# Kernel tuning notes

Measured on AMD Instinct MI355X. Metric: run time of the kernel, lower is better.

## Reference

```python
import jax, jax.numpy as jnp
import numpy as np

NEG_SLOPE = 0.2  # LeakyReLU slope

N, E, D_IN, D_OUT, H, NBIN = 50000, 500000, 256, 256, 8, 10
DH = D_OUT // H


def setup_inputs() -> dict:
    key = jax.random.key(0)
    ks = jax.random.split(key, 9)
    emb_rel = jax.random.normal(ks[0], (N, D_IN), dtype=jnp.float32)
    head_idxs = jax.random.randint(ks[1], (E,), 0, N, dtype=jnp.int32)
    tail_idxs = jax.random.randint(ks[2], (E,), 0, N, dtype=jnp.int32)
    bins = jax.random.randint(ks[3], (E,), 0, NBIN, dtype=jnp.int32)
    # xavier-normal-ish scaled params (gain for relu)
    attn_proj_w = jax.random.normal(ks[4], (D_OUT, 2 * D_IN), dtype=jnp.float32) * (1.4142 * (2.0 / (2 * D_IN + D_OUT)) ** 0.5)
    attn_proj_b = jnp.zeros((D_OUT,), dtype=jnp.float32)
    attn_bin = jax.random.normal(ks[5], (NBIN, H, 1), dtype=jnp.float32) * 0.3
    attn_vec = jax.random.normal(ks[6], (1, H, DH), dtype=jnp.float32) * (1.4142 * (2.0 / (H + DH)) ** 0.5)
    aggr_proj_w = jax.random.normal(ks[7], (D_OUT, D_IN), dtype=jnp.float32) * (1.4142 * (2.0 / (D_IN + D_OUT)) ** 0.5)
    aggr_proj_b = jnp.zeros((D_OUT,), dtype=jnp.float32)
    return {
        "emb_rel": emb_rel,
        "head_idxs": head_idxs,
        "tail_idxs": tail_idxs,
        "bins": bins,
        "attn_proj_w": attn_proj_w,
        "attn_proj_b": attn_proj_b,
        "attn_bin": attn_bin,
        "attn_vec": attn_vec,
        "aggr_proj_w": aggr_proj_w,
        "aggr_proj_b": aggr_proj_b,
        "num_nodes": N,
    }


def reference(emb_rel, head_idxs, tail_idxs, bins, attn_proj_w, attn_proj_b,
              attn_bin, attn_vec, aggr_proj_w, aggr_proj_b, num_nodes):
    num_head, dim_hid = attn_vec.shape[1], attn_vec.shape[2]
    eh = emb_rel[head_idxs]                      # (E, D_in)
    et = emb_rel[tail_idxs]                      # (E, D_in)
    concat = jnp.concatenate([eh, et], axis=-1)  # (E, 2*D_in)
    proj = (concat @ attn_proj_w.T + attn_proj_b).reshape(-1, num_head, dim_hid)
    lrelu = jnp.where(proj >= 0, proj, NEG_SLOPE * proj)
    # raw attention logits per edge/head: (E, H, 1)
    attn_raw = jnp.sum(lrelu * attn_vec, axis=-1, keepdims=True) + attn_bin[bins]
    # segmented softmax over edges grouped by head node
    seg_max = jax.ops.segment_max(attn_raw, head_idxs, num_segments=num_nodes)
    seg_max = jnp.where(jnp.isfinite(seg_max), seg_max, 0.0)  # empty segments -> 0 (never gathered anyway)
    attn_val = jnp.exp(attn_raw - seg_max[head_idxs])
    attn_sums = jax.ops.segment_sum(attn_val, head_idxs, num_segments=num_nodes)
    beta = attn_val / (attn_sums[head_idxs] + 1e-16)            # (E, H, 1)
    aggr = (et @ aggr_proj_w.T + aggr_proj_b).reshape(-1, num_head, dim_hid)
    out = jax.ops.segment_sum(beta * aggr, head_idxs, num_segments=num_nodes)
    return out.reshape(num_nodes, num_head * dim_hid)
```

## Files before the change

kernel.cpp:

```cpp
#include <hip/hip_runtime.h>
#include <math.h>

#define D_IN 256
#define D_OUT 256
#define NH 8
#define DH 32
#define NBIN 10
#define NEG_SLOPE 0.2f
#define CAP 96
#define LOG2E 1.4426950408889634f
#define THR 8.0f

typedef short short8 __attribute__((ext_vector_type(8)));
typedef float f32x4 __attribute__((ext_vector_type(4)));

__device__ __forceinline__ unsigned short f2bf(float f) {
  unsigned u = __float_as_uint(f);
  unsigned r = u + 0x7fffu + ((u >> 16) & 1u);
  return (unsigned short)(r >> 16);
}
__device__ __forceinline__ float bf2f(unsigned short s) {
  return __uint_as_float((unsigned)s << 16);
}

__device__ __forceinline__ void gload16(const void* g, void* l) {
  __builtin_amdgcn_global_load_lds(
      (const __attribute__((address_space(1))) unsigned int*)g,
      (__attribute__((address_space(3))) unsigned int*)l, 16, 0, 0);
}

__global__ void prep_kernel(const float* __restrict__ attn_w,
                            const float* __restrict__ attn_b,
                            const float* __restrict__ aggr_w,
                            const float* __restrict__ aggr_b,
                            const float* __restrict__ emb,
                            unsigned short* __restrict__ WCbf,
                            float* __restrict__ biasC,
                            unsigned short* __restrict__ embbf,
                            int* __restrict__ cnt, int N) {
  const int b = blockIdx.x, k = threadIdx.x;
  if (b < 768) {
    const int j = b;
    int idx0 = j * 256 + k;
    if (idx0 < N) cnt[idx0] = 0;
    float v, bia = 0.f;
    if (j < 256) {
      v = attn_w[j * 512 + k];
    } else {
      int idx = j - 256, g = idx >> 3, r = idx & 7;
      if (r < 4) { int c = g * 4 + r;     v = attn_w[c * 512 + 256 + k]; bia = attn_b[c]; }
      else       { int c = g * 4 + r - 4; v = aggr_w[c * 256 + k];       bia = aggr_b[c]; }
    }
    WCbf[j * 256 + k] = f2bf(v);
    if (k == 0) biasC[j] = bia;
  } else {
    const long long total = (long long)N * 256;
    long long i = (((long long)(b - 768)) * 256 + k) * 8;
    if (i >= total) return;
    float4 a = *(const float4*)(emb + i);
    float4 c = *(const float4*)(emb + i + 4);
    short8 o;
    o[0] = (short)f2bf(a.x); o[1] = (short)f2bf(a.y);
    o[2] = (short)f2bf(a.z); o[3] = (short)f2bf(a.w);
    o[4] = (short)f2bf(c.x); o[5] = (short)f2bf(c.y);
    o[6] = (short)f2bf(c.z); o[7] = (short)f2bf(c.w);
    *(short8*)(embbf + i) = o;
  }
}

#define EPAD 36
__global__ __launch_bounds__(256) void gemm_bf16_kernel(
    const unsigned short* __restrict__ Abf,
    const unsigned short* __restrict__ Bbf,
    const float* __restrict__ biasC,
    float* __restrict__ P1, unsigned short* __restrict__ P2A, int N) {
  __shared__ char smem[128 * EPAD * 4];
  unsigned short* As = (unsigned short*)smem;
  unsigned short* Bs = (unsigned short*)(smem + 8192);
  float* Ls = (float*)smem;
  const int tid = threadIdx.x;
  const int row0 = blockIdx.y * 128, col0 = blockIdx.x * 128;
  const int wave = tid >> 6, l = tid & 63;
  const int wm = wave >> 1, wn = wave & 1;
  const int lr = l & 15;
  const int lq = l >> 4;
  const int srow = tid >> 2;
  const int sk = (tid & 3) * 8;
  int ar0 = row0 + srow;      if (ar0 >= N) ar0 = N - 1;
  int ar1 = row0 + 64 + srow; if (ar1 >= N) ar1 = N - 1;
  const unsigned short* pa0 = Abf + (size_t)ar0 * 256 + sk;
  const unsigned short* pa1 = Abf + (size_t)ar1 * 256 + sk;
  const unsigned short* pb0 = Bbf + (size_t)(col0 + srow) * 256 + sk;
  const unsigned short* pb1 = Bbf + (size_t)(col0 + 64 + srow) * 256 + sk;
  unsigned short* lA0 = As + wave * 512;
  unsigned short* lA1 = As + 2048 + wave * 512;
  unsigned short* lB0 = Bs + wave * 512;
  unsigned short* lB1 = Bs + 2048 + wave * 512;
  f32x4 acc[4][4] = {};
  for (int kk = 0; kk < 256; kk += 32) {
    __syncthreads();
    gload16(pa0 + kk, lA0);
    gload16(pa1 + kk, lA1);
    gload16(pb0 + kk, lB0);
    gload16(pb1 + kk, lB1);
    __syncthreads();
    short8 af[4], bfr[4];
#pragma unroll
    for (int i = 0; i < 4; ++i)
      af[i] = *(const short8*)&As[(wm * 64 + i * 16 + lr) * 32 + lq * 8];
#pragma unroll
    for (int j = 0; j < 4; ++j)
      bfr[j] = *(const short8*)&Bs[(wn * 64 + j * 16 + lr) * 32 + lq * 8];
#pragma unroll
    for (int i = 0; i < 4; ++i)
#pragma unroll
      for (int j = 0; j < 4; ++j)
        acc[i][j] = __builtin_amdgcn_mfma_f32_16x16x32_bf16(af[i], bfr[j], acc[i][j], 0, 0, 0);
  }
  for (int j = 0; j < 4; ++j) {
    __syncthreads();
    const float bias = biasC[col0 + wn * 64 + j * 16 + lr];
#pragma unroll
    for (int i = 0; i < 4; ++i) {
      const int lrow = wm * 64 + i * 16 + lq * 4;
#pragma unroll
      for (int r = 0; r < 4; ++r)
        Ls[(lrow + r) * EPAD + wn * 16 + lr] = acc[i][j][r] + bias;
    }
    __syncthreads();
    if (col0 < 256) {
      const int sub = tid & 7, half = sub >> 2, quad = sub & 3;
#pragma unroll
      for (int s = 0; s < 4; ++s) {
        const int row = (tid >> 3) + s * 32;
        const int grow = row0 + row;
        if (grow < N) {
          float4 v = *(const float4*)&Ls[row * EPAD + half * 16 + quad * 4];
          *(float4*)(P1 + (size_t)grow * 256 + col0 + half * 64 + j * 16 + quad * 4) = v;
        }
      }
    } else {
      const int o = tid & 3, half = o >> 1, part = o & 1;
#pragma unroll
      for (int s = 0; s < 2; ++s) {
        const int row = (tid >> 2) + s * 64;
        const int grow = row0 + row;
        if (grow < N) {
          const float* src = &Ls[row * EPAD + half * 16 + part * 8];
          short8 v;
#pragma unroll
          for (int q = 0; q < 8; ++q) v[q] = (short)f2bf(src[q]);
          *(short8*)(P2A + (size_t)grow * 512 + (col0 - 256) + half * 64 + j * 16 + part * 8) = v;
        }
      }
    }
  }
}

__global__ void bucket_scatter_kernel(const int* __restrict__ head,
                                      const int* __restrict__ tail,
                                      const int* __restrict__ bins,
                                      int* __restrict__ cnt,
                                      int* __restrict__ bucket, int E) {
  int e = blockIdx.x * blockDim.x + threadIdx.x;
  if (e >= E) return;
  int h = head[e];
  int slot = atomicAdd(&cnt[h], 1);
  if (slot < CAP) bucket[(size_t)h * CAP + slot] = (bins[e] << 16) | tail[e];
}

template <int PAT>
__device__ __forceinline__ float swz_add(float s) {
  return s + __uint_as_float(
      (unsigned)__builtin_amdgcn_ds_swizzle((int)__float_as_uint(s), PAT));
}

__device__ __forceinline__ short8 ldP2A(const unsigned short* __restrict__ P2A,
                                        int t, int l8) {
  return *(const short8*)(P2A + ((size_t)(t & 0xFFFF) << 9) + l8);
}

__device__ __forceinline__ float edge_dot(short8 c, float4 p1, float4 av) {
  float x, s;
  x = p1.x + bf2f((unsigned short)c[0]); s  = fmaxf(x, NEG_SLOPE * x) * av.x;
  x = p1.y + bf2f((unsigned short)c[1]); s += fmaxf(x, NEG_SLOPE * x) * av.y;
  x = p1.z + bf2f((unsigned short)c[2]); s += fmaxf(x, NEG_SLOPE * x) * av.z;
  x = p1.w + bf2f((unsigned short)c[3]); s += fmaxf(x, NEG_SLOPE * x) * av.w;
  s = swz_add<0x041F>(s);
  s = swz_add<0x081F>(s);
  s = swz_add<0x101F>(s);
  return s;
}

__device__ __forceinline__ float4 edge_val(short8 c) {
  float4 v;
  v.x = bf2f((unsigned short)c[4]); v.y = bf2f((unsigned short)c[5]);
  v.z = bf2f((unsigned short)c[6]); v.w = bf2f((unsigned short)c[7]);
  return v;
}

__global__ __launch_bounds__(256) void node_aggr_kernel(
    const float* __restrict__ P1, const unsigned short* __restrict__ P2A,
    const int* __restrict__ cnt, const int* __restrict__ bucket,
    const float* __restrict__ attn_vec, const float* __restrict__ attn_bin,
    float* __restrict__ out, int N) {
  __shared__ float sbin[NBIN * NH];
  const int tid = threadIdx.x;
  if (tid < NBIN * NH) sbin[tid] = attn_bin[tid] * LOG2E;
  __syncthreads();
  const int nu = __builtin_amdgcn_readfirstlane(blockIdx.x * 4 + (tid >> 6));
  if (nu >= N) return;
  const int l = tid & 63;
  const int l8 = l * 8;
  const int h = l >> 3;
  float4 av = *(const float4*)(attn_vec + l * 4);
  av.x *= LOG2E; av.y *= LOG2E; av.z *= LOG2E; av.w *= LOG2E;
  const float4 p1 = *(const float4*)(P1 + (size_t)nu * 256 + l * 4);
  const int* brow = bucket + (size_t)nu * CAP;
  int d = cnt[nu];
  if (d > CAP) d = CAP;
  float m = 0.f, m8 = 0.f, sum = 0.f;
  float4 acc = make_float4(0.f, 0.f, 0.f, 0.f);
  if (d > 0) {
    const int dm1 = d - 1;
    const int t0 = brow[0];
    short8 c0 = ldP2A(P2A, t0, l8);
    int ta[4];
    short8 ca[4];
#pragma unroll
    for (int k = 0; k < 4; ++k) {
      const int ja = (1 + k <= dm1) ? 1 + k : dm1;
      ta[k] = brow[ja];
      ca[k] = ldP2A(P2A, ta[k], l8);
    }
    m = edge_dot(c0, p1, av) + sbin[(t0 >> 16) * NH + h];
    m8 = m + THR;
    sum = 1.f;
    const float4 v0 = edge_val(c0);
    acc.x = v0.x; acc.y = v0.y; acc.z = v0.z; acc.w = v0.w;
    int i = 1;
#pragma unroll 2
    for (; i + 3 < d; i += 4) {
      int tn[4];
      short8 cn[4];
#pragma unroll
      for (int k = 0; k < 4; ++k) {
        const int jn = (i + 4 + k <= dm1) ? i + 4 + k : dm1;
        tn[k] = brow[jn];
        cn[k] = ldP2A(P2A, tn[k], l8);
      }
      float lg[4];
#pragma unroll
      for (int k = 0; k < 4; ++k)
        lg[k] = edge_dot(ca[k], p1, av) + sbin[(ta[k] >> 16) * NH + h];
      const float lmax = fmaxf(fmaxf(lg[0], lg[1]), fmaxf(lg[2], lg[3]));
      if (__any(lmax > m8)) {
        const float mn = fmaxf(m, lmax);
        const float sc = __builtin_amdgcn_exp2f(m - mn);
        sum *= sc; acc.x *= sc; acc.y *= sc; acc.z *= sc; acc.w *= sc;
        m = mn; m8 = mn + THR;
      }
#pragma unroll
      for (int k = 0; k < 4; ++k) {
        const float w = __builtin_amdgcn_exp2f(lg[k] - m);
        const float4 v = edge_val(ca[k]);
        sum += w;
        acc.x += w * v.x; acc.y += w * v.y;
        acc.z += w * v.z; acc.w += w * v.w;
      }
#pragma unroll
      for (int k = 0; k < 4; ++k) { ta[k] = tn[k]; ca[k] = cn[k]; }
    }
    const int r = d - i;
#pragma unroll
    for (int k = 0; k < 3; ++k) {
      if (k < r) {
        const float lgk = edge_dot(ca[k], p1, av) + sbin[(ta[k] >> 16) * NH + h];
        if (__any(lgk > m8)) {
          const float mn = fmaxf(m, lgk);
          const float sc = __builtin_amdgcn_exp2f(m - mn);
          sum *= sc; acc.x *= sc; acc.y *= sc; acc.z *= sc; acc.w *= sc;
          m = mn; m8 = mn + THR;
        }
        const float w = __builtin_amdgcn_exp2f(lgk - m);
        const float4 v = edge_val(ca[k]);
        sum += w;
        acc.x += w * v.x; acc.y += w * v.y;
        acc.z += w * v.z; acc.w += w * v.w;
      }
    }
  }
  const float inv = 1.f / (sum + 1e-16f);
  float4 o;
  o.x = acc.x * inv; o.y = acc.y * inv; o.z = acc.z * inv; o.w = acc.w * inv;
  *(float4*)(out + (size_t)nu * 256 + l * 4) = o;
}

extern "C" void kernel_launch(void* const* d_in, const int* in_sizes, int n_in,
                              void* d_out, int out_size, void* d_ws, size_t ws_size,
                              hipStream_t stream) {
  const float* emb      = (const float*)d_in[0];
  const int*   head     = (const int*)d_in[1];
  const int*   tail     = (const int*)d_in[2];
  const int*   bins     = (const int*)d_in[3];
  const float* attn_w   = (const float*)d_in[4];
  const float* attn_b   = (const float*)d_in[5];
  const float* attn_bin = (const float*)d_in[6];
  const float* attn_vec = (const float*)d_in[7];
  const float* aggr_w   = (const float*)d_in[8];
  const float* aggr_b   = (const float*)d_in[9];
  float* out = (float*)d_out;

  const int N = in_sizes[0] / D_IN;
  const int E = in_sizes[1];

  char* ws = (char*)d_ws;
  size_t off = 0;
  auto walloc = [&](size_t bytes) -> void* {
    void* p = ws + off;
    off += (bytes + 255) & ~(size_t)255;
    return p;
  };
  float*          P1     = (float*)walloc((size_t)N * 256 * sizeof(float));
  unsigned short* P2A    = (unsigned short*)walloc((size_t)N * 512 * sizeof(short));
  unsigned short* embbf  = (unsigned short*)walloc((size_t)N * 256 * sizeof(short));
  unsigned short* WCbf   = (unsigned short*)walloc((size_t)768 * 256 * sizeof(short));
  float*          biasC  = (float*)walloc(768 * sizeof(float));
  int*            cnt    = (int*)walloc((size_t)N * sizeof(int));
  int*            bucket = (int*)walloc((size_t)N * CAP * sizeof(int));

  const int conv_blocks = (int)(((long long)N * 256 / 8 + 255) / 256);
  prep_kernel<<<768 + conv_blocks, 256, 0, stream>>>(attn_w, attn_b, aggr_w, aggr_b,
                                                     emb, WCbf, biasC, embbf, cnt, N);

  dim3 ggrid(768 / 128, (N + 127) / 128);
  gemm_bf16_kernel<<<ggrid, 256, 0, stream>>>(embbf, WCbf, biasC, P1, P2A, N);

  bucket_scatter_kernel<<<(E + 255) / 256, 256, 0, stream>>>(head, tail, bins, cnt, bucket, E);

  node_aggr_kernel<<<(N + 3) / 4, 256, 0, stream>>>(P1, P2A, cnt, bucket,
                                                    attn_vec, attn_bin, out, N);
}
```

Before: 290.5 us.

## Double-buffer GEMM LDS staging, swap grid order, shrink aggregation blocks

The bf16 GEMM now double-buffers its LDS tiles, prefetching the next K-slice while MFMAs run on the current one, and cuts the barriers per K step from two to one. The grid is transposed so row blocks vary fastest, which changes which blocks share the B tiles in cache. The node aggregation kernel moves to 128-thread blocks (2 nodes per block), and sched_barriers pin the gather loads ahead of the compute. The costs are doubled LDS use in the GEMM, which may lower occupancy, and more blocks to launch in the aggregation kernel.

```diff
diff --git a/kernel.cpp b/kernel.cpp
--- a/kernel.cpp
+++ b/kernel.cpp
@@ -74,12 +74,10 @@
     const unsigned short* __restrict__ Bbf,
     const float* __restrict__ biasC,
     float* __restrict__ P1, unsigned short* __restrict__ P2A, int N) {
-  __shared__ char smem[128 * EPAD * 4];
-  unsigned short* As = (unsigned short*)smem;
-  unsigned short* Bs = (unsigned short*)(smem + 8192);
+  __shared__ char smem[32768];
   float* Ls = (float*)smem;
   const int tid = threadIdx.x;
-  const int row0 = blockIdx.y * 128, col0 = blockIdx.x * 128;
+  const int row0 = blockIdx.x * 128, col0 = blockIdx.y * 128;
   const int wave = tid >> 6, l = tid & 63;
   const int wm = wave >> 1, wn = wave & 1;
   const int lr = l & 15;
@@ -92,18 +90,24 @@
   const unsigned short* pa1 = Abf + (size_t)ar1 * 256 + sk;
   const unsigned short* pb0 = Bbf + (size_t)(col0 + srow) * 256 + sk;
   const unsigned short* pb1 = Bbf + (size_t)(col0 + 64 + srow) * 256 + sk;
-  unsigned short* lA0 = As + wave * 512;
-  unsigned short* lA1 = As + 2048 + wave * 512;
-  unsigned short* lB0 = Bs + wave * 512;
-  unsigned short* lB1 = Bs + 2048 + wave * 512;
+
+  auto STAGE = [&](int buf, int kk) {
+    unsigned short* base = (unsigned short*)(smem + buf * 16384);
+    gload16(pa0 + kk, base + wave * 512);
+    gload16(pa1 + kk, base + 2048 + wave * 512);
+    gload16(pb0 + kk, base + 4096 + wave * 512);
+    gload16(pb1 + kk, base + 6144 + wave * 512);
+  };
+
   f32x4 acc[4][4] = {};
-  for (int kk = 0; kk < 256; kk += 32) {
-    __syncthreads();
-    gload16(pa0 + kk, lA0);
-    gload16(pa1 + kk, lA1);
-    gload16(pb0 + kk, lB0);
-    gload16(pb1 + kk, lB1);
-    __syncthreads();
+  STAGE(0, 0);
+  __syncthreads();
+  int cur = 0;
+  for (int t = 0; t < 8; ++t) {
+    if (t < 7) STAGE(cur ^ 1, (t + 1) * 32);
+    __builtin_amdgcn_sched_barrier(0);
+    const unsigned short* As = (const unsigned short*)(smem + cur * 16384);
+    const unsigned short* Bs = As + 4096;
     short8 af[4], bfr[4];
 #pragma unroll
     for (int i = 0; i < 4; ++i)
@@ -116,6 +120,8 @@
 #pragma unroll
       for (int j = 0; j < 4; ++j)
         acc[i][j] = __builtin_amdgcn_mfma_f32_16x16x32_bf16(af[i], bfr[j], acc[i][j], 0, 0, 0);
+    __syncthreads();
+    cur ^= 1;
   }
   for (int j = 0; j < 4; ++j) {
     __syncthreads();
@@ -199,7 +205,7 @@
   return v;
 }
 
-__global__ __launch_bounds__(256) void node_aggr_kernel(
+__global__ __launch_bounds__(128) void node_aggr_kernel(
     const float* __restrict__ P1, const unsigned short* __restrict__ P2A,
     const int* __restrict__ cnt, const int* __restrict__ bucket,
     const float* __restrict__ attn_vec, const float* __restrict__ attn_bin,
@@ -208,7 +214,7 @@
   const int tid = threadIdx.x;
   if (tid < NBIN * NH) sbin[tid] = attn_bin[tid] * LOG2E;
   __syncthreads();
-  const int nu = __builtin_amdgcn_readfirstlane(blockIdx.x * 4 + (tid >> 6));
+  const int nu = __builtin_amdgcn_readfirstlane(blockIdx.x * 2 + (tid >> 6));
   if (nu >= N) return;
   const int l = tid & 63;
   const int l8 = l * 8;
@@ -233,6 +239,7 @@
       ta[k] = brow[ja];
       ca[k] = ldP2A(P2A, ta[k], l8);
     }
+    __builtin_amdgcn_sched_barrier(0);
     m = edge_dot(c0, p1, av) + sbin[(t0 >> 16) * NH + h];
     m8 = m + THR;
     sum = 1.f;
@@ -249,6 +256,7 @@
         tn[k] = brow[jn];
         cn[k] = ldP2A(P2A, tn[k], l8);
       }
+      __builtin_amdgcn_sched_barrier(0);
       float lg[4];
 #pragma unroll
       for (int k = 0; k < 4; ++k)
@@ -333,11 +341,11 @@
   prep_kernel<<<768 + conv_blocks, 256, 0, stream>>>(attn_w, attn_b, aggr_w, aggr_b,
                                                      emb, WCbf, biasC, embbf, cnt, N);
 
-  dim3 ggrid(768 / 128, (N + 127) / 128);
+  dim3 ggrid((N + 127) / 128, 768 / 128);
   gemm_bf16_kernel<<<ggrid, 256, 0, stream>>>(embbf, WCbf, biasC, P1, P2A, N);
 
   bucket_scatter_kernel<<<(E + 255) / 256, 256, 0, stream>>>(head, tail, bins, cnt, bucket, E);
 
-  node_aggr_kernel<<<(N + 3) / 4, 256, 0, stream>>>(P1, P2A, cnt, bucket,
+  node_aggr_kernel<<<(N + 1) / 2, 128, 0, stream>>>(P1, P2A, cnt, bucket,
                                                     attn_vec, attn_bin, out, N);
 }
```

After: 294.8 us. Within noise of the previous version (+1.5%).
